# Kernel tuning notes

Hardware: AMD Instinct MI355X
Metric: run time of the kernel (lower is better)

## Reference

```python
import jax, jax.numpy as jnp
import numpy as np

# Static rendering config (from init_kwargs)
H, W, D = 128, 128, 64          # image height, width, depth samples
PIXEL = 1.0                      # pixel size
EXTENT_Z = 128.0
DZ = EXTENT_Z / D                # z spacing = 2.0
HIDDEN = 64                      # field MLP hidden dim
MD, MH, MW = 128, 128, 128       # mask volume shape


def _axis(n, s):
    # arange(n) - n/2 + 0.5, scaled: centered grid axis (center_grid_origin=True)
    return (jnp.arange(n, dtype=jnp.float32) - n / 2 + 0.5) * s


def make_base_grid():
    # cartesian_prod(px, py, pz, [1]) reshaped to [H, W, D, 4] == meshgrid 'ij'
    px, py, pz = _axis(H, PIXEL), _axis(W, PIXEL), _axis(D, DZ)
    gx, gy, gz = jnp.meshgrid(px, py, pz, indexing='ij')
    return jnp.stack([gx, gy, gz, jnp.ones_like(gx)], axis=-1)  # [H,W,D,4]


def trilinear_zeros(vol, xyz):
    """torch F.grid_sample 3D, bilinear, padding_mode='zeros', align_corners=True.
    vol: [Dm,Hm,Wm]; xyz: [N,3] normalized coords in [-1,1], x indexes W, y->H, z->D."""
    Dm, Hm, Wm = vol.shape
    x = (xyz[:, 0] + 1.0) * 0.5 * (Wm - 1)
    y = (xyz[:, 1] + 1.0) * 0.5 * (Hm - 1)
    z = (xyz[:, 2] + 1.0) * 0.5 * (Dm - 1)
    x0, y0, z0 = jnp.floor(x), jnp.floor(y), jnp.floor(z)
    fx, fy, fz = x - x0, y - y0, z - z0
    out = jnp.zeros_like(x)
    for dz_ in (0, 1):
        for dy_ in (0, 1):
            for dx_ in (0, 1):
                xi, yi, zi = x0 + dx_, y0 + dy_, z0 + dz_
                w = ((fx if dx_ else 1.0 - fx)
                     * (fy if dy_ else 1.0 - fy)
                     * (fz if dz_ else 1.0 - fz))
                valid = ((xi >= 0) & (xi <= Wm - 1) & (yi >= 0) & (yi <= Hm - 1)
                         & (zi >= 0) & (zi <= Dm - 1))
                v = vol[jnp.clip(zi, 0, Dm - 1).astype(jnp.int32),
                        jnp.clip(yi, 0, Hm - 1).astype(jnp.int32),
                        jnp.clip(xi, 0, Wm - 1).astype(jnp.int32)]
                out = out + w * jnp.where(valid, v, 0.0)
    return out


def setup_inputs() -> dict:
    key = jax.random.key(0)
    k1, k2, k3, k4 = jax.random.split(key, 4)
    # rigid rotation (last row [0,0,0,1]) so homogeneous w stays 1
    th, ph = 0.3, 0.5
    c, s = np.cos(th), np.sin(th)
    c2, s2 = np.cos(ph), np.sin(ph)
    Rz = np.array([[c, -s, 0, 0], [s, c, 0, 0], [0, 0, 1, 0], [0, 0, 0, 1]], np.float32)
    Rx = np.array([[1, 0, 0, 0], [0, c2, -s2, 0], [0, s2, c2, 0], [0, 0, 0, 1]], np.float32)
    T = jnp.asarray(Rz @ Rx)[None]  # [1,4,4]
    mask_vol = (jax.random.uniform(k1, (MD, MH, MW)) > 0.4).astype(jnp.float32)
    W1 = jax.random.normal(k2, (3, HIDDEN), jnp.float32) * 0.5
    b1 = jax.random.normal(k3, (HIDDEN,), jnp.float32) * 0.1
    W2 = jax.random.normal(k4, (HIDDEN, 1), jnp.float32) * 0.2
    b2 = jnp.zeros((1,), jnp.float32)
    return {"transform_matrix": T, "mask_vol": mask_vol,
            "W1": W1, "b1": b1, "W2": W2, "b2": b2}


def reference(transform_matrix, mask_vol, W1, b1, W2, b2):
    base = make_base_grid().reshape(-1, 4)           # [N,4], N = H*W*D
    T = transform_matrix[0]                          # [4,4]
    q = base @ T.T                                   # transformed homogeneous points [N,4]
    # setup_masked_buffers: normalize to [-1,1] by max |coord| of the base grid
    max_abs = jnp.max(jnp.abs(base[:, :3]))
    norm_xyz = q[:, :3] / max_abs
    m_interp = trilinear_zeros(mask_vol, norm_xyz)   # trilinear mask sample [N]
    mask = (m_interp != 0).astype(jnp.float32)       # .to(torch.bool) cast
    # forward: homogeneous divide, field eval (masked points only; here mask-weighted)
    q3 = q[:, :3] / q[:, 3:4]                        # [N,3]
    h = jax.nn.relu(q3 @ W1 + b1)                    # [N,HIDDEN]
    pot = (h @ W2 + b2)[:, 0]                        # [N]
    # segment_sum_csr over contiguous depth bins == sum over z axis per pixel
    img = jnp.sum((pot * mask).reshape(H, W, D), axis=-1) * DZ  # [H,W]
    return img[None]                                 # [1,H,W] (batch 1)
```

## Files before the change

### kernel.cpp

```cpp
#include <hip/hip_runtime.h>


#define NH 128
#define NW 128
#define ND 64
#define HID 64

__global__ __launch_bounds__(256) void pack_kernel(
    const float* __restrict__ vol,
    unsigned long long* __restrict__ bits)
{
    const int t = blockIdx.x * 256 + threadIdx.x;
    const float v = vol[t];
    const unsigned long long b = __ballot(v != 0.0f);
    if ((threadIdx.x & 63) == 0)
        bits[t >> 6] = b;
}

__global__ __launch_bounds__(256) void dilate_kernel(
    const unsigned long long* __restrict__ b,
    unsigned long long* __restrict__ oc)
{
    const int r = blockIdx.x * 256 + threadIdx.x;
    const int z = r >> 7, y = r & 127;
    const int i = r << 1;
    unsigned long long lo = b[i], hi = b[i + 1];
    if (y < 127) { lo |= b[i + 2];   hi |= b[i + 3]; }
    if (z < 127) {
        lo |= b[i + 256]; hi |= b[i + 257];
        if (y < 127) { lo |= b[i + 258]; hi |= b[i + 259]; }
    }
    oc[i]     = lo | (lo >> 1) | (hi << 63);
    oc[i + 1] = hi | (hi >> 1);
}

__global__ __launch_bounds__(256) void dmp_kernel(
    const float* __restrict__ T,
    const unsigned int* __restrict__ bw,
    const unsigned int* __restrict__ oc,
    const float* __restrict__ W1,
    const float* __restrict__ b1,
    const float* __restrict__ W2,
    const float* __restrict__ b2,
    float* __restrict__ out)
{
    const int t    = blockIdx.x * 256 + threadIdx.x;
    const int lane = t & 63;
    const int pix  = t >> 6;
    const int h    = pix >> 7;
    const int w    = pix & 127;

    const float bx = (float)h - 63.5f;
    const float by = (float)w - 63.5f;
    const float bz = ((float)lane - 31.5f) * 2.0f;

    const float q0 = T[0] * bx + T[1] * by + T[2]  * bz + T[3];
    const float q1 = T[4] * bx + T[5] * by + T[6]  * bz + T[7];
    const float q2 = T[8] * bx + T[9] * by + T[10] * bz + T[11];

    const float inv_max = 1.0f / 63.5f;
    const float xf = (q0 * inv_max + 1.0f) * 0.5f * 127.0f;
    const float yf = (q1 * inv_max + 1.0f) * 0.5f * 127.0f;
    const float zf = (q2 * inv_max + 1.0f) * 0.5f * 127.0f;
    const float x0 = floorf(xf), y0 = floorf(yf), z0 = floorf(zf);
    const float fx = xf - x0, fy = yf - y0, fz = zf - z0;

    const bool lane_touch = (xf >= -1.0f) && (x0 <= 127.0f)
                         && (yf >= -1.0f) && (y0 <= 127.0f)
                         && (zf >= -1.0f) && (z0 <= 127.0f);

    const bool generic = (x0 >= 0.0f) && (x0 <= 126.0f) && (fx != 0.0f)
                      && (y0 >= 0.0f) && (y0 <= 126.0f) && (fy != 0.0f)
                      && (z0 >= 0.0f) && (z0 <= 126.0f) && (fz != 0.0f);

    const int x0i = (int)x0, y0i = (int)y0, z0i = (int)z0;
    const int xg = min(max(x0i, 0), 127);
    const int yg = min(max(y0i, 0), 127);
    const int zg = min(max(z0i, 0), 127);
    const unsigned int ocw = oc[((zg << 7) + yg) * 4 + (xg >> 5)];
    const bool ocbit = (ocw >> (xg & 31)) & 1u;

    float m = 0.0f;
    const bool edge = lane_touch && !generic;
    if (__any(edge)) {
        #pragma unroll
        for (int dz_ = 0; dz_ < 2; ++dz_) {
            #pragma unroll
            for (int dy_ = 0; dy_ < 2; ++dy_) {
                #pragma unroll
                for (int dx_ = 0; dx_ < 2; ++dx_) {
                    const float xi = x0 + (float)dx_;
                    const float yi = y0 + (float)dy_;
                    const float zi = z0 + (float)dz_;
                    const float wgt = (dx_ ? fx : 1.0f - fx)
                                    * (dy_ ? fy : 1.0f - fy)
                                    * (dz_ ? fz : 1.0f - fz);
                    const bool valid = (xi >= 0.0f) && (xi <= 127.0f)
                                    && (yi >= 0.0f) && (yi <= 127.0f)
                                    && (zi >= 0.0f) && (zi <= 127.0f);
                    const int xc = min(max((int)xi, 0), 127);
                    const int yc = min(max((int)yi, 0), 127);
                    const int zc = min(max((int)zi, 0), 127);
                    const unsigned int word = bw[((zc << 7) + yc) * 4 + (xc >> 5)];
                    const bool bit = (word >> (xc & 31)) & 1u;
                    m += (edge && valid && bit) ? wgt : 0.0f;
                }
            }
        }
    }
    const bool masked = generic ? ocbit : (m != 0.0f);
    const unsigned long long M = __ballot(masked);

    if (M == 0ull) {
        if (lane == 0) out[pix] = 0.0f;
        return;
    }

    const int j = lane;
    const float w0 = W1[j], w1 = W1[64 + j], w2 = W1[128 + j];
    const float A  = w0 * T[0] + w1 * T[4] + w2 * T[8];
    const float B  = w0 * T[1] + w1 * T[5] + w2 * T[9];
    const float C  = w0 * T[2] + w1 * T[6] + w2 * T[10];
    const float D0 = w0 * T[3] + w1 * T[7] + w2 * T[11] + b1[j];
    const float u  = A * bx + B * by - 63.0f * C + D0;
    const float g  = C + C;

    unsigned long long rmask;
    if (g > 0.0f) {
        const float tt = __fdividef(-u, g);
        int d0 = (int)floorf(tt) + 1;
        d0 = min(max(d0, 0), 64);
        if (d0 > 0 && fmaf(g, (float)(d0 - 1), u) > 0.0f)       d0 -= 1;
        else if (d0 < 64 && fmaf(g, (float)d0, u) <= 0.0f)      d0 += 1;
        rmask = (d0 >= 64) ? 0ull : (~0ull << d0);
    } else if (g < 0.0f) {
        const float tt = __fdividef(-u, g);
        int d1 = (int)floorf(tt);
        d1 = min(max(d1, -1), 63);
        if (d1 < 63 && fmaf(g, (float)(d1 + 1), u) > 0.0f)      d1 += 1;
        else if (d1 >= 0 && fmaf(g, (float)d1, u) <= 0.0f)      d1 -= 1;
        rmask = (d1 < 0) ? 0ull : (~0ull >> (63 - d1));
    } else {
        rmask = (u > 0.0f) ? ~0ull : 0ull;
    }

    const unsigned long long R = rmask & M;
    const unsigned int rlo = (unsigned int)R;
    const unsigned int rhi = (unsigned int)(R >> 32);
    const int N = __popc(rlo) + __popc(rhi);
    int Dsum = __popc(rlo & 0xAAAAAAAAu)        + (__popc(rlo & 0xCCCCCCCCu) << 1)
             + (__popc(rlo & 0xF0F0F0F0u) << 2) + (__popc(rlo & 0xFF00FF00u) << 3)
             + (__popc(rlo & 0xFFFF0000u) << 4);
    Dsum += __popc(rhi & 0xAAAAAAAAu)        + (__popc(rhi & 0xCCCCCCCCu) << 1)
          + (__popc(rhi & 0xF0F0F0F0u) << 2) + (__popc(rhi & 0xFF00FF00u) << 3)
          + (__popc(rhi & 0xFFFF0000u) << 4) + (__popc(rhi) << 5);

    const float S = u * (float)N + g * (float)Dsum;
    float val = W2[j] * S;

    #pragma unroll
    for (int off = 32; off > 0; off >>= 1)
        val += __shfl_down(val, off);

    if (lane == 0) {
        const float nm = (float)(__popc((unsigned int)M)
                               + __popc((unsigned int)(M >> 32)));
        out[pix] = (val + b2[0] * nm) * 2.0f;
    }
}

extern "C" void kernel_launch(void* const* d_in, const int* in_sizes, int n_in,
                              void* d_out, int out_size, void* d_ws, size_t ws_size,
                              hipStream_t stream) {
    const float* T   = (const float*)d_in[0];
    const float* vol = (const float*)d_in[1];
    const float* W1  = (const float*)d_in[2];
    const float* b1  = (const float*)d_in[3];
    const float* W2  = (const float*)d_in[4];
    const float* b2  = (const float*)d_in[5];
    float* out = (float*)d_out;

    unsigned long long* bits = (unsigned long long*)d_ws;
    unsigned long long* oc   = (unsigned long long*)((char*)d_ws + 262144);

    pack_kernel<<<8192, 256, 0, stream>>>(vol, bits);
    dilate_kernel<<<64, 256, 0, stream>>>(bits, oc);

    const int n_points = NH * NW * ND;
    dmp_kernel<<<n_points / 256, 256, 0, stream>>>(
        T, (const unsigned int*)bits, (const unsigned int*)oc,
        W1, b1, W2, b2, out);
}
```

Before: 89.03 us.

## Fuse x-dilation into pack kernel and drop separate dilate pass

Removes the separate dilate kernel launch and instead writes an x-dilated, padded bitmask (256 bits per row) straight from the pack kernel through shared memory. In exchange, the main kernel now does four bitmask lookups per point (one for each y/z neighbor) to decide occupancy, and falls back to the exact trilinear weighting only when a fractional coordinate is exactly zero. This removes one launch and one dependent pass but adds gather loads in the hot kernel and a block-wide synchronization in the pack kernel.

Result: faster. 80.77 us (-9.3%).

```diff
diff --git a/kernel.cpp b/kernel.cpp
--- a/kernel.cpp
+++ b/kernel.cpp
@@ -6,38 +6,33 @@
 #define ND 64
 #define HID 64
 
-__global__ __launch_bounds__(256) void pack_kernel(
+__global__ __launch_bounds__(256) void pack_xdil_kernel(
     const float* __restrict__ vol,
-    unsigned long long* __restrict__ bits)
+    unsigned long long* __restrict__ bits,
+    unsigned long long* __restrict__ xd)
 {
+    __shared__ unsigned long long s[4];
     const int t = blockIdx.x * 256 + threadIdx.x;
     const float v = vol[t];
     const unsigned long long b = __ballot(v != 0.0f);
-    if ((threadIdx.x & 63) == 0)
-        bits[t >> 6] = b;
-}
-
-__global__ __launch_bounds__(256) void dilate_kernel(
-    const unsigned long long* __restrict__ b,
-    unsigned long long* __restrict__ oc)
-{
-    const int r = blockIdx.x * 256 + threadIdx.x;
-    const int z = r >> 7, y = r & 127;
-    const int i = r << 1;
-    unsigned long long lo = b[i], hi = b[i + 1];
-    if (y < 127) { lo |= b[i + 2];   hi |= b[i + 3]; }
-    if (z < 127) {
-        lo |= b[i + 256]; hi |= b[i + 257];
-        if (y < 127) { lo |= b[i + 258]; hi |= b[i + 259]; }
+    if ((threadIdx.x & 63) == 0) s[threadIdx.x >> 6] = b;
+    __syncthreads();
+    if (threadIdx.x < 2) {
+        const int r = blockIdx.x * 2 + threadIdx.x;
+        const unsigned long long lo = s[threadIdx.x * 2];
+        const unsigned long long hi = s[threadIdx.x * 2 + 1];
+        bits[r * 2]     = lo;
+        bits[r * 2 + 1] = hi;
+        xd[r * 4]     = lo | (lo << 1);
+        xd[r * 4 + 1] = hi | (hi << 1) | (lo >> 63);
+        xd[r * 4 + 2] = hi >> 63;
     }
-    oc[i]     = lo | (lo >> 1) | (hi << 63);
-    oc[i + 1] = hi | (hi >> 1);
 }
 
 __global__ __launch_bounds__(256) void dmp_kernel(
     const float* __restrict__ T,
     const unsigned int* __restrict__ bw,
-    const unsigned int* __restrict__ oc,
+    const unsigned int* __restrict__ xd,
     const float* __restrict__ W1,
     const float* __restrict__ b1,
     const float* __restrict__ W2,
@@ -69,20 +64,27 @@
                          && (yf >= -1.0f) && (y0 <= 127.0f)
                          && (zf >= -1.0f) && (z0 <= 127.0f);
 
-    const bool generic = (x0 >= 0.0f) && (x0 <= 126.0f) && (fx != 0.0f)
-                      && (y0 >= 0.0f) && (y0 <= 126.0f) && (fy != 0.0f)
-                      && (z0 >= 0.0f) && (z0 <= 126.0f) && (fz != 0.0f);
+    const int x0i = (int)x0, y0i = (int)y0, z0i = (int)z0;
+    const int xI  = min(max(x0i + 1, 0), 128);
+    bool masked = false;
+    #pragma unroll
+    for (int dz_ = 0; dz_ < 2; ++dz_) {
+        #pragma unroll
+        for (int dy_ = 0; dy_ < 2; ++dy_) {
+            const int zr = z0i + dz_;
+            const int yr = y0i + dy_;
+            const bool vzy = (zr >= 0) && (zr <= 127) && (yr >= 0) && (yr <= 127);
+            const int zc = min(max(zr, 0), 127);
+            const int yc = min(max(yr, 0), 127);
+            const unsigned int word = xd[(((zc << 7) + yc) << 3) + (xI >> 5)];
+            masked = masked || (vzy && (((word >> (xI & 31)) & 1u) != 0u));
+        }
+    }
+    masked = masked && lane_touch;
 
-    const int x0i = (int)x0, y0i = (int)y0, z0i = (int)z0;
-    const int xg = min(max(x0i, 0), 127);
-    const int yg = min(max(y0i, 0), 127);
-    const int zg = min(max(z0i, 0), 127);
-    const unsigned int ocw = oc[((zg << 7) + yg) * 4 + (xg >> 5)];
-    const bool ocbit = (ocw >> (xg & 31)) & 1u;
-
-    float m = 0.0f;
-    const bool edge = lane_touch && !generic;
-    if (__any(edge)) {
+    const bool fb = lane_touch && ((fx == 0.0f) || (fy == 0.0f) || (fz == 0.0f));
+    if (__any(fb)) {
+        float m = 0.0f;
         #pragma unroll
         for (int dz_ = 0; dz_ < 2; ++dz_) {
             #pragma unroll
@@ -103,14 +105,14 @@
                     const int zc = min(max((int)zi, 0), 127);
                     const unsigned int word = bw[((zc << 7) + yc) * 4 + (xc >> 5)];
                     const bool bit = (word >> (xc & 31)) & 1u;
-                    m += (edge && valid && bit) ? wgt : 0.0f;
+                    m += (fb && valid && bit) ? wgt : 0.0f;
                 }
             }
         }
+        if (fb) masked = (m != 0.0f);
     }
-    const bool masked = generic ? ocbit : (m != 0.0f);
+
     const unsigned long long M = __ballot(masked);
-
     if (M == 0ull) {
         if (lane == 0) out[pix] = 0.0f;
         return;
@@ -181,13 +183,12 @@
     float* out = (float*)d_out;
 
     unsigned long long* bits = (unsigned long long*)d_ws;
-    unsigned long long* oc   = (unsigned long long*)((char*)d_ws + 262144);
+    unsigned long long* xd   = (unsigned long long*)((char*)d_ws + 262144);
 
-    pack_kernel<<<8192, 256, 0, stream>>>(vol, bits);
-    dilate_kernel<<<64, 256, 0, stream>>>(bits, oc);
+    pack_xdil_kernel<<<8192, 256, 0, stream>>>(vol, bits, xd);
 
     const int n_points = NH * NW * ND;
     dmp_kernel<<<n_points / 256, 256, 0, stream>>>(
-        T, (const unsigned int*)bits, (const unsigned int*)oc,
+        T, (const unsigned int*)bits, (const unsigned int*)xd,
         W1, b1, W2, b2, out);
 }
```
